# Optimization experiments

Hardware: AMD Instinct MI355X
Metric: run time of the kernel (lower is better)

The kernel has to match this reference:

```python
import jax, jax.numpy as jnp
import numpy as np

TAU = 2.0       # init_tau
VTH = 1.0       # v_threshold
VRESET = 0.0    # v_reset (hard reset)
ALPHA = 2.0     # ATan surrogate width
H = 8           # num_heads
W = 20          # attention_window
TIME_STEP = 2   # config.time_step -> global_scale uses 1000 // time_step


@jax.custom_vjp
def spike(x):
    return (x >= 0.0).astype(x.dtype)

def _spike_fwd(x):
    return (x >= 0.0).astype(x.dtype), x

def _spike_bwd(x, g):
    # ATan surrogate gradient (spikingjelly default)
    sg = (ALPHA / 2.0) / (1.0 + (jnp.pi / 2.0 * ALPHA * x) ** 2)
    return (g * sg,)

spike.defvjp(_spike_fwd, _spike_bwd)


def lif(x_seq):
    """Multi-step LIF, decay_input=False, hard reset. x_seq: [T, ...] -> spikes [T, ...]."""
    def step(v, x):
        h = v - (v - VRESET) / TAU + x          # neuronal charge (decay_input=False)
        s = spike(h - VTH)
        v_new = s * VRESET + (1.0 - s) * h      # hard reset
        return v_new, s
    _, s_seq = jax.lax.scan(step, jnp.zeros_like(x_seq[0]), x_seq)
    return s_seq


def bn(x, gamma, beta, eps=1e-5):
    # BatchNorm1d step_mode='m': stats over (T, B) per channel (training-mode stats)
    mean = x.mean(axis=(0, 1))
    var = x.var(axis=(0, 1))
    return (x - mean) * jax.lax.rsqrt(var + eps) * gamma + beta


def _shift(a, o):
    # a: [B, H, T, D]; out[..., t, :] = a[..., t + o, :], zero outside -> local band
    if o == 0:
        return a
    B_, H_, T_, D_ = a.shape
    z = jnp.zeros((B_, H_, abs(o), D_), a.dtype)
    if o > 0:
        return jnp.concatenate([a[:, :, o:, :], z], axis=2)
    return jnp.concatenate([z, a[:, :, :o, :]], axis=2)


def _forward(x, wq, wk, wv, w_mattn, w_proj, w_dw, w_pw, bn_gamma, bn_beta):
    T, B, C = x.shape
    D = C // H
    local_scale = 1.0 / np.sqrt(D * (2 * W + 1)).astype(np.float32)
    global_scale = 1.0 / np.sqrt(D * (1000 // TIME_STEP)).astype(np.float32)

    # spiking QKV: pointwise conv (kernel 1) + BN + LIF
    q = lif(bn(jnp.einsum('tbc,dc->tbd', x, wq), bn_gamma[0], bn_beta[0]))
    k = lif(bn(jnp.einsum('tbc,dc->tbd', x, wk), bn_gamma[1], bn_beta[1]))
    v = lif(bn(jnp.einsum('tbc,dc->tbd', x, wv), bn_gamma[2], bn_beta[2]))

    heads = lambda a: a.reshape(T, B, H, D).transpose(1, 2, 0, 3)   # [B,H,T,D]
    unheads = lambda a: a.transpose(2, 0, 1, 3).reshape(T, B, C)    # [T,B,C]
    qh, kh, vh = heads(q), heads(k), heads(v)

    # global spiking self-attention (no softmax): (Q K^T) V * global_scale
    attn = jnp.einsum('bhtd,bhsd->bhts', qh, kh)
    g_spk = lif(unheads(jnp.einsum('bhts,bhsd->bhtd', attn, vh) * global_scale))

    # local sliding-window attention over offsets [-W, W] (banded, no [T,T] matrix)
    out_l = jnp.zeros_like(vh)
    for o in range(-W, W + 1):
        s = jnp.einsum('bhtd,bhtd->bht', qh, _shift(kh, o))
        out_l = out_l + s[..., None] * _shift(vh, o)
    l_spk = lif(unheads(out_l * local_scale))

    # depthwise temporal conv branch on V: v_dw -> LIF -> v_pw (1x1 over heads)
    dw = jax.lax.conv_general_dilated(
        vh, w_dw, window_strides=(1, 1), padding=((4, 4), (0, 0)),
        dimension_numbers=('NCHW', 'OIHW', 'NCHW'), feature_group_count=H)
    dw_spk_h = heads(lif(unheads(dw)))
    dw_out = unheads(jnp.einsum('bhtd,gh->bgtd', dw_spk_h, w_pw))

    # merge branches, then mattn conv+BN+LIF and proj conv+BN+LIF
    y0 = lif(g_spk + l_spk + dw_out)
    y1 = lif(bn(jnp.einsum('tbc,dc->tbd', y0, w_mattn), bn_gamma[3], bn_beta[3]))
    out = lif(bn(jnp.einsum('tbc,dc->tbd', y1, w_proj), bn_gamma[4], bn_beta[4]))
    return out


def setup_inputs() -> dict:
    key = jax.random.key(0)
    ks = jax.random.split(key, 10)
    T, B, C = 500, 8, 512
    sc = 0.03
    x = jax.random.normal(ks[0], (T, B, C), jnp.float32)
    wq = jax.random.normal(ks[1], (C, C), jnp.float32) * sc
    wk = jax.random.normal(ks[2], (C, C), jnp.float32) * sc
    wv = jax.random.normal(ks[3], (C, C), jnp.float32) * sc
    w_mattn = jax.random.normal(ks[4], (C, C), jnp.float32) * sc
    w_proj = jax.random.normal(ks[5], (C, C), jnp.float32) * sc
    w_dw = jax.random.normal(ks[6], (H, 1, 9, 1), jnp.float32) * 0.3   # depthwise (9,1)
    w_pw = jax.random.normal(ks[7], (H, H), jnp.float32) * 0.3         # 1x1 over heads
    bn_gamma = jax.random.uniform(ks[8], (5, C), jnp.float32) + 0.5
    bn_beta = jax.random.normal(ks[9], (5, C), jnp.float32) * 0.1
    return {'x': x, 'wq': wq, 'wk': wk, 'wv': wv, 'w_mattn': w_mattn,
            'w_proj': w_proj, 'w_dw': w_dw, 'w_pw': w_pw,
            'bn_gamma': bn_gamma, 'bn_beta': bn_beta}


def reference(x, wq, wk, wv, w_mattn, w_proj, w_dw, w_pw, bn_gamma, bn_beta):
    return _forward(x, wq, wk, wv, w_mattn, w_proj, w_dw, w_pw, bn_gamma, bn_beta)
```

## Files before the change

### kernel.cpp

```cpp
#include <hip/hip_runtime.h>
#include <cmath>

#define TT 500
#define NTOT 2048000
#define WW 20

typedef _Float16 f16x8 __attribute__((ext_vector_type(8)));
typedef _Float16 f16x4 __attribute__((ext_vector_type(4)));
typedef float f32x4 __attribute__((ext_vector_type(4)));

#define C1SC 4.8828125e-4f
#define C2SC 2.384185791015625e-7f

__device__ __forceinline__ void gload16(const _Float16* g, _Float16* l) {
    __builtin_amdgcn_global_load_lds(
        (const __attribute__((address_space(1))) unsigned int*)g,
        (__attribute__((address_space(3))) unsigned int*)l, 16, 0, 0);
}

__global__ __launch_bounds__(256) void prep_split_k(
    const float* __restrict__ x, const float* __restrict__ wq,
    const float* __restrict__ wk, const float* __restrict__ wv,
    const float* __restrict__ wm, const float* __restrict__ wp,
    _Float16* __restrict__ X0, _Float16* __restrict__ X1, _Float16* __restrict__ X2,
    _Float16* __restrict__ Q0, _Float16* __restrict__ Q1, _Float16* __restrict__ Q2,
    _Float16* __restrict__ M0, _Float16* __restrict__ M1, _Float16* __restrict__ M2,
    _Float16* __restrict__ P0, _Float16* __restrict__ P1, _Float16* __restrict__ P2)
{
    int gid = blockIdx.x * 256 + threadIdx.x;
    const float* src;
    _Float16 *d0, *d1, *d2;
    size_t si, di;
    if (gid < 512000) {
        src = x; d0 = X0; d1 = X1; d2 = X2; si = di = (size_t)gid * 4;
    } else if (gid < 708608) {
        int g = gid - 512000;
        int s3 = g >> 16;
        src = (s3 == 0) ? wq : ((s3 == 1) ? wk : wv);
        d0 = Q0; d1 = Q1; d2 = Q2;
        si = (size_t)(g & 65535) * 4;
        di = (size_t)g * 4;
    } else if (gid < 774144) {
        int g = gid - 708608;
        src = wm; d0 = M0; d1 = M1; d2 = M2; si = di = (size_t)g * 4;
    } else {
        int g = gid - 774144;
        src = wp; d0 = P0; d1 = P1; d2 = P2; si = di = (size_t)g * 4;
    }
    float4 v = *(const float4*)(src + si);
    float f[4] = {v.x, v.y, v.z, v.w};
    f16x4 a, b, c;
#pragma unroll
    for (int i = 0; i < 4; ++i) {
        _Float16 h0 = (_Float16)f[i];
        float r1 = f[i] - (float)h0;
        _Float16 h1 = (_Float16)(r1 * 2048.0f);
        float r2 = r1 - (float)h1 * C1SC;
        _Float16 h2 = (_Float16)(r2 * 4194304.0f);
        a[i] = h0; b[i] = h1; c[i] = h2;
    }
    *(f16x4*)(d0 + di) = a;
    *(f16x4*)(d1 + di) = b;
    *(f16x4*)(d2 + di) = c;
}

__global__ __launch_bounds__(256) void gemm_f16s3_k(
    const _Float16* __restrict__ X0, const _Float16* __restrict__ X1,
    const _Float16* __restrict__ X2,
    const _Float16* __restrict__ B0g, const _Float16* __restrict__ B1g,
    const _Float16* __restrict__ B2g,
    float* __restrict__ out, float* __restrict__ colpart, int M)
{
    __shared__ __align__(16) _Float16 sA[36864];
    int tid = threadIdx.x;
    int bid = blockIdx.x;
    int xcd = bid & 7;
    int j = bid >> 3;
    int mblk = (xcd << 3) | (j & 7);
    int nblk = j >> 3;
    int mBase = mblk * 64;
    int nBase = nblk * 128;
    int wv = tid >> 6;
    int lane = tid & 63;
    int wr = wv >> 1, wc = wv & 1;
    int lg = lane >> 4, l16 = lane & 15;

    int subrow = lane >> 2;
    int s4 = lane & 3;
    int rA = (wv << 4) + subrow;
    int sl8 = (s4 ^ ((rA >> 1) & 3)) * 8;
    int mA = mBase + rA; if (mA >= M) mA = 0;
    const _Float16* gA0 = X0 + (size_t)mA * 512 + sl8;
    const _Float16* gA1 = X1 + (size_t)mA * 512 + sl8;
    const _Float16* gA2 = X2 + (size_t)mA * 512 + sl8;
    const _Float16* gB00 = B0g + (size_t)(nBase + rA) * 512 + sl8;
    const _Float16* gB01 = B0g + (size_t)(nBase + 64 + rA) * 512 + sl8;
    const _Float16* gB10 = B1g + (size_t)(nBase + rA) * 512 + sl8;
    const _Float16* gB11 = B1g + (size_t)(nBase + 64 + rA) * 512 + sl8;
    const _Float16* gB20 = B2g + (size_t)(nBase + rA) * 512 + sl8;
    const _Float16* gB21 = B2g + (size_t)(nBase + 64 + rA) * 512 + sl8;
    int wb = wv << 9;
    _Float16* lA0 = sA + wb;
    _Float16* lA1 = sA + 2048 + wb;
    _Float16* lA2 = sA + 4096 + wb;
    _Float16* lB00 = sA + 6144 + wb;
    _Float16* lB01 = sA + 8192 + wb;
    _Float16* lB10 = sA + 10240 + wb;
    _Float16* lB11 = sA + 12288 + wb;
    _Float16* lB20 = sA + 14336 + wb;
    _Float16* lB21 = sA + 16384 + wb;

    auto stage = [&](int kt, int off) {
        gload16(gA0 + kt, lA0 + off);
        gload16(gA1 + kt, lA1 + off);
        gload16(gA2 + kt, lA2 + off);
        gload16(gB00 + kt, lB00 + off);
        gload16(gB01 + kt, lB01 + off);
        gload16(gB10 + kt, lB10 + off);
        gload16(gB11 + kt, lB11 + off);
        gload16(gB20 + kt, lB20 + off);
        gload16(gB21 + kt, lB21 + off);
    };

    int sd = (lg ^ ((l16 >> 1) & 3)) * 8;

    f32x4 acc0[2][4] = {}, acc1[2][4] = {}, acc2[2][4] = {};

    stage(0, 0);
    __syncthreads();
    int cur = 0;
    for (int kt = 0; kt < 512; kt += 32) {
        int coff = cur * 18432;
        if (kt + 32 < 512) stage(kt + 32, 18432 - coff);
        f16x8 a0f[2], a1f[2], a2f[2];
#pragma unroll
        for (int i = 0; i < 2; ++i) {
            int off = (wr * 32 + i * 16 + l16) * 32 + sd + coff;
            a0f[i] = *(const f16x8*)&sA[off];
            a1f[i] = *(const f16x8*)&sA[2048 + off];
            a2f[i] = *(const f16x8*)&sA[4096 + off];
        }
#pragma unroll
        for (int jj = 0; jj < 4; ++jj) {
            int boff = 6144 + (wc * 64 + jj * 16 + l16) * 32 + sd + coff;
            f16x8 b0f = *(const f16x8*)&sA[boff];
            f16x8 b1f = *(const f16x8*)&sA[4096 + boff];
            f16x8 b2f = *(const f16x8*)&sA[8192 + boff];
#pragma unroll
            for (int i = 0; i < 2; ++i) {
                acc0[i][jj] = __builtin_amdgcn_mfma_f32_16x16x32_f16(a0f[i], b0f, acc0[i][jj], 0, 0, 0);
                acc1[i][jj] = __builtin_amdgcn_mfma_f32_16x16x32_f16(a0f[i], b1f, acc1[i][jj], 0, 0, 0);
                acc1[i][jj] = __builtin_amdgcn_mfma_f32_16x16x32_f16(a1f[i], b0f, acc1[i][jj], 0, 0, 0);
                acc2[i][jj] = __builtin_amdgcn_mfma_f32_16x16x32_f16(a1f[i], b1f, acc2[i][jj], 0, 0, 0);
                acc2[i][jj] = __builtin_amdgcn_mfma_f32_16x16x32_f16(a0f[i], b2f, acc2[i][jj], 0, 0, 0);
                acc2[i][jj] = __builtin_amdgcn_mfma_f32_16x16x32_f16(a2f[i], b0f, acc2[i][jj], 0, 0, 0);
            }
        }
        __syncthreads();
        cur ^= 1;
    }
#pragma unroll
    for (int i = 0; i < 2; ++i)
#pragma unroll
        for (int jj = 0; jj < 4; ++jj)
#pragma unroll
            for (int r = 0; r < 4; ++r)
                acc0[i][jj][r] = fmaf(C2SC, acc2[i][jj][r],
                                      fmaf(C1SC, acc1[i][jj][r], acc0[i][jj][r]));
    float* red = (float*)sA;
#pragma unroll
    for (int jj = 0; jj < 4; ++jj) {
        float s = 0.f, q = 0.f;
#pragma unroll
        for (int i = 0; i < 2; ++i)
#pragma unroll
            for (int r = 0; r < 4; ++r) {
                int mrow = mBase + wr * 32 + i * 16 + lg * 4 + r;
                float v = (mrow < M) ? acc0[i][jj][r] : 0.f;
                s += v; q = fmaf(v, v, q);
            }
        s += __shfl_xor(s, 16, 64); s += __shfl_xor(s, 32, 64);
        q += __shfl_xor(q, 16, 64); q += __shfl_xor(q, 32, 64);
        if (lane < 16) {
            int col = wc * 64 + jj * 16 + lane;
            red[(wr * 128 + col) * 2 + 0] = s;
            red[(wr * 128 + col) * 2 + 1] = q;
        }
    }
    __syncthreads();
    if (tid < 128) {
        float ss = red[tid * 2 + 0] + red[(128 + tid) * 2 + 0];
        float qq = red[tid * 2 + 1] + red[(128 + tid) * 2 + 1];
        colpart[((size_t)mblk * 1536 + nBase + tid) * 2 + 0] = ss;
        colpart[((size_t)mblk * 1536 + nBase + tid) * 2 + 1] = qq;
    }
    int wsel = nBase >> 9;
    int col0 = nBase & 511;
    float* outp = out + (size_t)wsel * NTOT;
#pragma unroll
    for (int i = 0; i < 2; ++i) {
        int m0 = mBase + wr * 32 + i * 16 + lg * 4;
#pragma unroll
        for (int jj = 0; jj < 4; ++jj) {
            int cc = col0 + wc * 64 + jj * 16 + l16;
#pragma unroll
            for (int r = 0; r < 4; ++r) {
                int m = m0 + r;
                if (m < M) outp[(size_t)m * 512 + cc] = acc0[i][jj][r];
            }
        }
    }
}

__global__ __launch_bounds__(256) void gemm_hs3_k(
    const _Float16* __restrict__ Ah,
    const _Float16* __restrict__ B0g, const _Float16* __restrict__ B1g,
    const _Float16* __restrict__ B2g,
    float* __restrict__ out, float* __restrict__ colpart, int M)
{
    __shared__ __align__(16) _Float16 sH[16384];
    int tid = threadIdx.x;
    int bid = blockIdx.x;
    int xcd = bid & 7;
    int j = bid >> 3;
    int mblk = (xcd << 3) | (j & 7);
    int nblk = j >> 3;
    int mBase = mblk * 64;
    int col0 = nblk * 64;
    int wv = tid >> 6;
    int lane = tid & 63;
    int wr = wv >> 1, wc = wv & 1;
    int lg = lane >> 4, l16 = lane & 15;

    int subrow = lane >> 2;
    int s4 = lane & 3;
    int rA = (wv << 4) + subrow;
    int sl8 = (s4 ^ ((rA >> 1) & 3)) * 8;
    int mA = mBase + rA; if (mA >= M) mA = 0;
    const _Float16* gA  = Ah  + (size_t)mA * 512 + sl8;
    const _Float16* gB0 = B0g + (size_t)(col0 + rA) * 512 + sl8;
    const _Float16* gB1 = B1g + (size_t)(col0 + rA) * 512 + sl8;
    const _Float16* gB2 = B2g + (size_t)(col0 + rA) * 512 + sl8;
    int wb = wv << 9;
    _Float16* lA  = sH + wb;
    _Float16* lB0 = sH + 2048 + wb;
    _Float16* lB1 = sH + 4096 + wb;
    _Float16* lB2 = sH + 6144 + wb;

    auto stage = [&](int kt, int off) {
        gload16(gA + kt, lA + off);
        gload16(gB0 + kt, lB0 + off);
        gload16(gB1 + kt, lB1 + off);
        gload16(gB2 + kt, lB2 + off);
    };

    int sd = (lg ^ ((l16 >> 1) & 3)) * 8;

    f32x4 acc0[2][2] = {}, acc1[2][2] = {}, acc2[2][2] = {};

    stage(0, 0);
    __syncthreads();
    int cur = 0;
    for (int kt = 0; kt < 512; kt += 32) {
        int coff = cur * 8192;
        if (kt + 32 < 512) stage(kt + 32, 8192 - coff);
        f16x8 af[2];
#pragma unroll
        for (int i = 0; i < 2; ++i)
            af[i] = *(const f16x8*)&sH[(wr * 32 + i * 16 + l16) * 32 + sd + coff];
#pragma unroll
        for (int jj = 0; jj < 2; ++jj) {
            int boff = 2048 + (wc * 32 + jj * 16 + l16) * 32 + sd + coff;
            f16x8 b0f = *(const f16x8*)&sH[boff];
            f16x8 b1f = *(const f16x8*)&sH[2048 + boff];
            f16x8 b2f = *(const f16x8*)&sH[4096 + boff];
#pragma unroll
            for (int i = 0; i < 2; ++i) {
                acc0[i][jj] = __builtin_amdgcn_mfma_f32_16x16x32_f16(af[i], b0f, acc0[i][jj], 0, 0, 0);
                acc1[i][jj] = __builtin_amdgcn_mfma_f32_16x16x32_f16(af[i], b1f, acc1[i][jj], 0, 0, 0);
                acc2[i][jj] = __builtin_amdgcn_mfma_f32_16x16x32_f16(af[i], b2f, acc2[i][jj], 0, 0, 0);
            }
        }
        __syncthreads();
        cur ^= 1;
    }
#pragma unroll
    for (int i = 0; i < 2; ++i)
#pragma unroll
        for (int jj = 0; jj < 2; ++jj)
#pragma unroll
            for (int r = 0; r < 4; ++r)
                acc0[i][jj][r] = fmaf(C2SC, acc2[i][jj][r],
                                      fmaf(C1SC, acc1[i][jj][r], acc0[i][jj][r]));
    float* red = (float*)sH;
#pragma unroll
    for (int jj = 0; jj < 2; ++jj) {
        float s = 0.f, q = 0.f;
#pragma unroll
        for (int i = 0; i < 2; ++i)
#pragma unroll
            for (int r = 0; r < 4; ++r) {
                int mrow = mBase + wr * 32 + i * 16 + lg * 4 + r;
                float v = (mrow < M) ? acc0[i][jj][r] : 0.f;
                s += v; q = fmaf(v, v, q);
            }
        s += __shfl_xor(s, 16, 64); s += __shfl_xor(s, 32, 64);
        q += __shfl_xor(q, 16, 64); q += __shfl_xor(q, 32, 64);
        if (lane < 16) {
            int col = wc * 32 + jj * 16 + lane;
            red[(wr * 64 + col) * 2 + 0] = s;
            red[(wr * 64 + col) * 2 + 1] = q;
        }
    }
    __syncthreads();
    if (tid < 64) {
        float ss = red[tid * 2 + 0] + red[(64 + tid) * 2 + 0];
        float qq = red[tid * 2 + 1] + red[(64 + tid) * 2 + 1];
        colpart[((size_t)mblk * 512 + col0 + tid) * 2 + 0] = ss;
        colpart[((size_t)mblk * 512 + col0 + tid) * 2 + 1] = qq;
    }
#pragma unroll
    for (int i = 0; i < 2; ++i) {
        int m0 = mBase + wr * 32 + i * 16 + lg * 4;
#pragma unroll
        for (int jj = 0; jj < 2; ++jj) {
            int cc = col0 + wc * 32 + jj * 16 + l16;
#pragma unroll
            for (int r = 0; r < 4; ++r) {
                int m = m0 + r;
                if (m < M) out[(size_t)m * 512 + cc] = acc0[i][jj][r];
            }
        }
    }
}

__global__ __launch_bounds__(256) void lif_seg_k(
    const float* __restrict__ pre, const float* __restrict__ colpart, int CT, int chunks,
    const float* __restrict__ gamma, const float* __restrict__ beta,
    float* __restrict__ outF, unsigned char* __restrict__ outB,
    _Float16* __restrict__ outH, int segLen, int warm)
{
    int gid = blockIdx.x * 256 + threadIdx.x;
    int tensor = gid >> 12;
    int bc = gid & 4095;
    int ch = (tensor << 9) | (bc & 511);
    double s = 0.0, s2 = 0.0;
    for (int k = 0; k < chunks; ++k) {
        s  += (double)colpart[((size_t)k * CT + ch) * 2 + 0];
        s2 += (double)colpart[((size_t)k * CT + ch) * 2 + 1];
    }
    double mean = s / 4000.0;
    double var = s2 / 4000.0 - mean * mean;
    double scd = (double)gamma[ch] / sqrt(var + 1e-5);
    float sc = (float)scd;
    float sh = (float)((double)beta[ch] - mean * scd);
    const float* q0 = pre + (size_t)tensor * NTOT + bc;
    float* oF = outF ? outF + (size_t)tensor * NTOT + bc : nullptr;
    unsigned char* oB = outB ? outB + (size_t)tensor * NTOT + bc : nullptr;
    _Float16* oH = outH ? outH + (size_t)tensor * NTOT + bc : nullptr;
    int t0 = blockIdx.y * segLen;
    int twarm = (t0 - warm > 0) ? (t0 - warm) : 0;
    int tend = (t0 + segLen < TT) ? (t0 + segLen) : TT;
    float v = 0.f;
    float b0[8];
#pragma unroll
    for (int j = 0; j < 8; ++j) {
        int tt = twarm + j;
        b0[j] = (tt < tend) ? q0[(size_t)tt * 4096] : 0.f;
    }
    for (int t = twarm; t < tend; t += 8) {
        float n0[8];
#pragma unroll
        for (int j = 0; j < 8; ++j) {
            int tt = t + 8 + j;
            n0[j] = (tt < tend) ? q0[(size_t)tt * 4096] : 0.f;
        }
#pragma unroll
        for (int j = 0; j < 8; ++j) {
            int tc = t + j;
            if (tc >= tend) break;
            float bnx = fmaf(b0[j], sc, sh);
            float h = fmaf(0.5f, v, bnx);
            float sp = (h >= 1.f) ? 1.f : 0.f;
            v = (h >= 1.f) ? 0.f : h;
            if (tc >= t0) {
                if (oB)      oB[(size_t)tc * 4096] = (unsigned char)sp;
                else if (oH) oH[(size_t)tc * 4096] = (_Float16)sp;
                else         oF[(size_t)tc * 4096] = sp;
            }
        }
#pragma unroll
        for (int j = 0; j < 8; ++j) b0[j] = n0[j];
    }
}

__global__ __launch_bounds__(256) void ktv_part_k(
    const unsigned char* __restrict__ kspk, const unsigned char* __restrict__ vspk,
    float* __restrict__ part)
{
    __shared__ __align__(16) float kb[16][64], vb[16][64];
    int bh = blockIdx.x;
    int seg = blockIdx.y;
    int t0p = seg * 125, t1p = t0p + 125;
    int b = bh >> 3, h = bh & 7;
    int tid = threadIdx.x;
    int d1b = (tid >> 4) * 4, d2b = (tid & 15) * 4;
    size_t cb = (size_t)b * 512 + h * 64;
    int sRow = tid >> 4;
    int sD = (tid & 15) * 4;
    float acc[4][4] = {};
    uchar4 pk, pv;
    auto preload = [&](int tt) {
        int t = tt + sRow;
        if (t < t1p) {
            pk = *(const uchar4*)(kspk + (size_t)t * 4096 + cb + sD);
            pv = *(const uchar4*)(vspk + (size_t)t * 4096 + cb + sD);
        } else {
            pk = make_uchar4(0, 0, 0, 0); pv = make_uchar4(0, 0, 0, 0);
        }
    };
    preload(t0p);
    for (int tt = t0p; tt < t1p; tt += 16) {
        __syncthreads();
        kb[sRow][sD + 0] = (float)pk.x; kb[sRow][sD + 1] = (float)pk.y;
        kb[sRow][sD + 2] = (float)pk.z; kb[sRow][sD + 3] = (float)pk.w;
        vb[sRow][sD + 0] = (float)pv.x; vb[sRow][sD + 1] = (float)pv.y;
        vb[sRow][sD + 2] = (float)pv.z; vb[sRow][sD + 3] = (float)pv.w;
        __syncthreads();
        preload(tt + 16);
#pragma unroll
        for (int tl = 0; tl < 16; ++tl) {
            float4 k4 = *(const float4*)&kb[tl][d1b];
            float4 v4 = *(const float4*)&vb[tl][d2b];
            float ka[4] = {k4.x, k4.y, k4.z, k4.w};
            float va[4] = {v4.x, v4.y, v4.z, v4.w};
#pragma unroll
            for (int i = 0; i < 4; ++i)
#pragma unroll
                for (int j = 0; j < 4; ++j)
                    acc[i][j] = fmaf(ka[i], va[j], acc[i][j]);
        }
    }
    size_t ob = ((size_t)seg * 64 + bh) * 4096;
#pragma unroll
    for (int i = 0; i < 4; ++i)
        *(float4*)(part + ob + (size_t)(d1b + i) * 64 + d2b) =
            make_float4(acc[i][0], acc[i][1], acc[i][2], acc[i][3]);
}

__global__ __launch_bounds__(256) void ktv_reduce_k(
    const float* __restrict__ part, float* __restrict__ ktv)
{
    int i4 = (blockIdx.x * 256 + threadIdx.x) * 4;
    float4 a = *(const float4*)(part + i4);
    float4 b = *(const float4*)(part + 262144 + i4);
    float4 c = *(const float4*)(part + 2 * 262144 + i4);
    float4 d = *(const float4*)(part + 3 * 262144 + i4);
    *(float4*)(ktv + i4) = make_float4(((a.x + b.x) + c.x) + d.x,
                                       ((a.y + b.y) + c.y) + d.y,
                                       ((a.z + b.z) + c.z) + d.z,
                                       ((a.w + b.w) + c.w) + d.w);
}

__global__ __launch_bounds__(256) void gapply_t_k(
    const unsigned char* __restrict__ sq, const float* __restrict__ ktv,
    float* __restrict__ gpre, float gscale)
{
    __shared__ float qs[10][512];
    int tid = threadIdx.x;
    int t0 = blockIdx.x * 10;
    int b = blockIdx.y;
    for (int i = tid; i < 1280; i += 256) {
        int t = i >> 7;
        int c4 = (i & 127) * 4;
        uchar4 u = *(const uchar4*)(sq + (size_t)(t0 + t) * 4096 + b * 512 + c4);
        qs[t][c4 + 0] = (float)u.x; qs[t][c4 + 1] = (float)u.y;
        qs[t][c4 + 2] = (float)u.z; qs[t][c4 + 3] = (float)u.w;
    }
    __syncthreads();
#pragma unroll
    for (int half = 0; half < 2; ++half) {
        int c = tid + half * 256;
        int h = c >> 6, dcol = c & 63;
        const float* kt = ktv + ((size_t)(b * 8 + h) * 64) * 64 + dcol;
        float acc[10] = {};
        for (int d1 = 0; d1 < 64; ++d1) {
            float kv = kt[(size_t)d1 * 64];
#pragma unroll
            for (int t = 0; t < 10; ++t)
                acc[t] = fmaf(qs[t][h * 64 + d1], kv, acc[t]);
        }
#pragma unroll
        for (int t = 0; t < 10; ++t)
            gpre[(size_t)(t0 + t) * 4096 + b * 512 + c] = acc[t] * gscale;
    }
}

__global__ __launch_bounds__(256) void local_k(
    const unsigned char* __restrict__ qspk, const unsigned char* __restrict__ kspk,
    const unsigned char* __restrict__ vspk, float* __restrict__ lpre, float lscale)
{
    __shared__ __align__(16) float qs[32][68];
    __shared__ __align__(16) float ks[72][68];
    __shared__ __align__(16) float vs[72][68];
    __shared__ float sm[32][72];
    int t0 = blockIdx.x * 32;
    int bh = blockIdx.y;
    int b = bh >> 3, h = bh & 7;
    int tid = threadIdx.x;
    size_t cb = (size_t)b * 512 + h * 64;

    for (int i = tid; i < 512; i += 256) {
        int r = i >> 4, d4 = (i & 15) * 4;
        int t = t0 + r;
        if (t < TT) {
            uchar4 u = *(const uchar4*)(qspk + (size_t)t * 4096 + cb + d4);
            qs[r][d4 + 0] = (float)u.x; qs[r][d4 + 1] = (float)u.y;
            qs[r][d4 + 2] = (float)u.z; qs[r][d4 + 3] = (float)u.w;
        } else {
            qs[r][d4 + 0] = 0.f; qs[r][d4 + 1] = 0.f; qs[r][d4 + 2] = 0.f; qs[r][d4 + 3] = 0.f;
        }
    }
    for (int i = tid; i < 1152; i += 256) {
        int r = i >> 4, d4 = (i & 15) * 4;
        int u_ = t0 - WW + r;
        if (u_ >= 0 && u_ < TT) {
            uchar4 uk = *(const uchar4*)(kspk + (size_t)u_ * 4096 + cb + d4);
            uchar4 uv = *(const uchar4*)(vspk + (size_t)u_ * 4096 + cb + d4);
            ks[r][d4 + 0] = (float)uk.x; ks[r][d4 + 1] = (float)uk.y;
            ks[r][d4 + 2] = (float)uk.z; ks[r][d4 + 3] = (float)uk.w;
            vs[r][d4 + 0] = (float)uv.x; vs[r][d4 + 1] = (float)uv.y;
            vs[r][d4 + 2] = (float)uv.z; vs[r][d4 + 3] = (float)uv.w;
        } else {
            ks[r][d4 + 0] = 0.f; ks[r][d4 + 1] = 0.f; ks[r][d4 + 2] = 0.f; ks[r][d4 + 3] = 0.f;
            vs[r][d4 + 0] = 0.f; vs[r][d4 + 1] = 0.f; vs[r][d4 + 2] = 0.f; vs[r][d4 + 3] = 0.f;
        }
    }
    __syncthreads();

    int tA = tid >> 3;
    int ug = tid & 7;
    float4 qreg[16];
#pragma unroll
    for (int i = 0; i < 16; ++i) qreg[i] = *(const float4*)&qs[tA][i * 4];
#pragma unroll
    for (int ui = 0; ui < 9; ++ui) {
        int u = ug + ui * 8;
        float acc = 0.f;
#pragma unroll
        for (int i = 0; i < 16; ++i) {
            float4 k4 = *(const float4*)&ks[u][i * 4];
            acc = fmaf(qreg[i].x, k4.x, acc);
            acc = fmaf(qreg[i].y, k4.y, acc);
            acc = fmaf(qreg[i].z, k4.z, acc);
            acc = fmaf(qreg[i].w, k4.w, acc);
        }
        sm[tA][u] = acc;
    }
    __syncthreads();

#pragma unroll
    for (int oi = 0; oi < 2; ++oi) {
        int idx = tid + oi * 256;
        int t = idx >> 4;
        int dg = (idx & 15) * 4;
        float4 acc = make_float4(0.f, 0.f, 0.f, 0.f);
        for (int o = 0; o < 41; ++o) {
            int u = t + o;
            float s = sm[t][u];
            float4 v4 = *(const float4*)&vs[u][dg];
            acc.x = fmaf(s, v4.x, acc.x);
            acc.y = fmaf(s, v4.y, acc.y);
            acc.z = fmaf(s, v4.z, acc.z);
            acc.w = fmaf(s, v4.w, acc.w);
        }
        int tg = t0 + t;
        if (tg < TT) {
            acc.x *= lscale; acc.y *= lscale; acc.z *= lscale; acc.w *= lscale;
            *(float4*)(lpre + (size_t)tg * 4096 + cb + dg) = acc;
        }
    }
}

__global__ __launch_bounds__(256) void branch_y0_k(
    const float* __restrict__ gpre, const float* __restrict__ lpre,
    const unsigned char* __restrict__ sv, const float* __restrict__ wdw,
    const float* __restrict__ wpw, _Float16* __restrict__ sy0,
    int segLen, int warm)
{
    int tid = threadIdx.x;
    int wave = tid >> 6, lane = tid & 63;
    int gw = blockIdx.x * 4 + wave;
    int b = gw >> 3, dg = gw & 7;
    int h = lane >> 3, dl = lane & 7;
    int c = h * 64 + dg * 8 + dl;
    int base = b * 512 + c;
    float w9[9];
#pragma unroll
    for (int j = 0; j < 9; ++j) w9[j] = wdw[h * 9 + j];
    float w8[8];
#pragma unroll
    for (int j = 0; j < 8; ++j) w8[j] = wpw[h * 8 + j];
    int t0 = blockIdx.y * segLen;
    int twarm = (t0 - warm > 0) ? (t0 - warm) : 0;
    int tend = (t0 + segLen < TT) ? (t0 + segLen) : TT;
    float vg = 0.f, vl = 0.f, vd = 0.f, vy = 0.f;
    float win[12];
#pragma unroll
    for (int i = 0; i < 12; ++i) {
        int tt = twarm - 4 + i;
        win[i] = (tt >= 0 && tt < TT) ? (float)sv[(size_t)tt * 4096 + base] : 0.f;
    }
    float pg[4], pl[4], pv[4];
    auto pref = [&](int t) {
#pragma unroll
        for (int j = 0; j < 4; ++j) {
            int tt = t + j;
            bool in = tt < tend;
            pg[j] = in ? gpre[(size_t)tt * 4096 + base] : 0.f;
            pl[j] = in ? lpre[(size_t)tt * 4096 + base] : 0.f;
            int tv = t + 8 + j;
            pv[j] = (tv < TT) ? (float)sv[(size_t)tv * 4096 + base] : 0.f;
        }
    };
    pref(twarm);
    for (int t = twarm; t < tend; t += 4) {
        float cg[4], cl[4], cv[4];
#pragma unroll
        for (int j = 0; j < 4; ++j) { cg[j] = pg[j]; cl[j] = pl[j]; cv[j] = pv[j]; }
        pref(t + 4);
#pragma unroll
        for (int j = 0; j < 4; ++j) {
            int tc = t + j;
            if (tc >= tend) break;
            float x = 0.f;
#pragma unroll
            for (int q = 0; q < 9; ++q) x = fmaf(w9[q], win[j + q], x);
            float hd = fmaf(0.5f, vd, x);
            float sd = (hd >= 1.f) ? 1.f : 0.f;
            vd = (hd >= 1.f) ? 0.f : hd;
            float hg = fmaf(0.5f, vg, cg[j]);
            float sg = (hg >= 1.f) ? 1.f : 0.f;
            vg = (hg >= 1.f) ? 0.f : hg;
            float hl = fmaf(0.5f, vl, cl[j]);
            float sl = (hl >= 1.f) ? 1.f : 0.f;
            vl = (hl >= 1.f) ? 0.f : hl;
            float mix = 0.f;
#pragma unroll
            for (int h2 = 0; h2 < 8; ++h2)
                mix = fmaf(w8[h2], __shfl(sd, h2 * 8 + dl, 64), mix);
            float xy = (sg + sl) + mix;
            float hy = fmaf(0.5f, vy, xy);
            float sy = (hy >= 1.f) ? 1.f : 0.f;
            vy = (hy >= 1.f) ? 0.f : hy;
            if (tc >= t0) sy0[(size_t)tc * 4096 + base] = (_Float16)sy;
        }
#pragma unroll
        for (int i = 0; i < 8; ++i) win[i] = win[i + 4];
#pragma unroll
        for (int i = 0; i < 4; ++i) win[8 + i] = cv[i];
    }
}

extern "C" void kernel_launch(void* const* d_in, const int* in_sizes, int n_in,
                              void* d_out, int out_size, void* d_ws, size_t ws_size,
                              hipStream_t stream)
{
    const float* x       = (const float*)d_in[0];
    const float* wq      = (const float*)d_in[1];
    const float* wk      = (const float*)d_in[2];
    const float* wv      = (const float*)d_in[3];
    const float* w_mattn = (const float*)d_in[4];
    const float* w_proj  = (const float*)d_in[5];
    const float* w_dw    = (const float*)d_in[6];
    const float* w_pw    = (const float*)d_in[7];
    const float* bn_g    = (const float*)d_in[8];
    const float* bn_b    = (const float*)d_in[9];
    float* out = (float*)d_out;
    float* ws = (float*)d_ws;

    float gs32 = (float)std::sqrt((double)(64 * 500));
    float gscale = (float)(1.0 / (double)gs32);
    float ls32 = (float)std::sqrt((double)(64 * 41));
    float lscale = (float)(1.0 / (double)ls32);
    const int M = TT * 8;

    float* S0 = ws;
    float* S1 = ws + (size_t)NTOT;
    float* S2 = ws + 2 * (size_t)NTOT;
    float* part4   = ws + 3 * (size_t)NTOT;
    float* ktvBuf  = part4 + 4 * 262144;
    float* colpart = ktvBuf + 262144;
    unsigned char* spk = (unsigned char*)(colpart + 196608);
    unsigned char* sq  = spk;
    unsigned char* sk  = spk + (size_t)NTOT;
    unsigned char* sv  = spk + 2 * (size_t)NTOT;
    _Float16* sy0h = (_Float16*)(spk + 3 * (size_t)NTOT);
    _Float16* sy1h = (_Float16*)spk;
    _Float16* X0 = (_Float16*)spk;
    _Float16* X1 = X0 + (size_t)NTOT;
    _Float16* X2 = X1 + (size_t)NTOT;
    _Float16* Wm0 = (_Float16*)(spk + 6 * (size_t)NTOT);
    _Float16* Wm1 = Wm0 + 262144;
    _Float16* Wm2 = Wm1 + 262144;
    _Float16* Wp0 = Wm2 + 262144;
    _Float16* Wp1 = Wp0 + 262144;
    _Float16* Wp2 = Wp1 + 262144;
    _Float16* Wq0 = (_Float16*)part4;
    _Float16* Wq1 = Wq0 + 786432;
    _Float16* Wq2 = Wq1 + 786432;

    prep_split_k<<<3280, 256, 0, stream>>>(x, wq, wk, wv, w_mattn, w_proj,
                                           X0, X1, X2, Wq0, Wq1, Wq2,
                                           Wm0, Wm1, Wm2, Wp0, Wp1, Wp2);
    gemm_f16s3_k<<<768, 256, 0, stream>>>(X0, X1, X2, Wq0, Wq1, Wq2, S0, colpart, M);
    lif_seg_k<<<dim3(48, 10), 256, 0, stream>>>(S0, colpart, 1536, 64, bn_g, bn_b,
                                                nullptr, sq, nullptr, 50, 64);
    ktv_part_k<<<dim3(64, 4), 256, 0, stream>>>(sk, sv, part4);
    ktv_reduce_k<<<256, 256, 0, stream>>>(part4, ktvBuf);
    gapply_t_k<<<dim3(50, 8), 256, 0, stream>>>(sq, ktvBuf, S0, gscale);
    local_k<<<dim3(16, 64), 256, 0, stream>>>(sq, sk, sv, S1, lscale);
    branch_y0_k<<<dim3(16, 20), 256, 0, stream>>>(S0, S1, sv, w_dw, w_pw, sy0h, 25, 64);
    gemm_hs3_k<<<512, 256, 0, stream>>>(sy0h, Wm0, Wm1, Wm2, S2, colpart, M);
    lif_seg_k<<<dim3(16, 20), 256, 0, stream>>>(S2, colpart, 512, 64, bn_g + 1536,
                                                bn_b + 1536, nullptr, nullptr, sy1h, 25, 64);
    gemm_hs3_k<<<512, 256, 0, stream>>>(sy1h, Wp0, Wp1, Wp2, S0, colpart, M);
    lif_seg_k<<<dim3(16, 20), 256, 0, stream>>>(S0, colpart, 512, 64, bn_g + 2048,
                                                bn_b + 2048, out, nullptr, nullptr, 25, 64);

    (void)in_sizes; (void)n_in; (void)out_size; (void)ws_size;
}
```

Measured before the change: 331.7 us.

## Stage branch_y0 inputs through double-buffered LDS via async global-to-LDS loads

Replaces the per-thread register prefetch of gpre, lpre and spike values in branch_y0_k with cooperative global_load_lds staging into double-buffered shared memory, eight timesteps at a time, using a swizzled column mapping so each load is wide and contiguous. The goal is to turn strided 4-byte per-lane loads into 16-byte vectorized transfers and overlap the next chunk's loads with the current sequential LIF recurrence. It adds block-wide barriers each chunk and extra LDS use, and the window update now shifts one element per step. The staged loads may read past tend or TT at the tail, which could touch out-of-range addresses.

```diff
diff --git a/kernel.cpp b/kernel.cpp
--- a/kernel.cpp
+++ b/kernel.cpp
@@ -16,6 +16,16 @@
     __builtin_amdgcn_global_load_lds(
         (const __attribute__((address_space(1))) unsigned int*)g,
         (__attribute__((address_space(3))) unsigned int*)l, 16, 0, 0);
+}
+__device__ __forceinline__ void gload16f(const float* g, float* l) {
+    __builtin_amdgcn_global_load_lds(
+        (const __attribute__((address_space(1))) unsigned int*)g,
+        (__attribute__((address_space(3))) unsigned int*)l, 16, 0, 0);
+}
+__device__ __forceinline__ void gload4b(const unsigned char* g, unsigned char* l) {
+    __builtin_amdgcn_global_load_lds(
+        (const __attribute__((address_space(1))) unsigned int*)g,
+        (__attribute__((address_space(3))) unsigned int*)l, 4, 0, 0);
 }
 
 __global__ __launch_bounds__(256) void prep_split_k(
@@ -588,13 +598,32 @@
     const float* __restrict__ wpw, _Float16* __restrict__ sy0,
     int segLen, int warm)
 {
+    __shared__ __align__(16) float gb[2][8][256];
+    __shared__ __align__(16) float lb[2][8][256];
+    __shared__ __align__(16) unsigned char vbuf[2][8][256];
     int tid = threadIdx.x;
     int wave = tid >> 6, lane = tid & 63;
-    int gw = blockIdx.x * 4 + wave;
-    int b = gw >> 3, dg = gw & 7;
+    int gw0 = blockIdx.x * 4;
+    int b = gw0 >> 3;
+    int dg0 = gw0 & 7;
     int h = lane >> 3, dl = lane & 7;
+    int dg = dg0 + wave;
     int c = h * 64 + dg * 8 + dl;
     int base = b * 512 + c;
+    int p = h * 32 + (((wave + h) & 3) << 3) + dl;
+
+    int rowS[2], gcol[2];
+#pragma unroll
+    for (int v = 0; v < 2; ++v) {
+        int f = tid + (v << 8);
+        rowS[v] = f >> 6;
+        int jj = f & 63;
+        int hj = jj >> 3;
+        int sj = (jj >> 1) & 3;
+        int wj = (sj - hj) & 3;
+        gcol[v] = b * 512 + hj * 64 + dg0 * 8 + (wj << 3) + ((jj & 1) << 2);
+    }
+
     float w9[9];
 #pragma unroll
     for (int j = 0; j < 9; ++j) w9[j] = wdw[h * 9 + j];
@@ -604,6 +633,25 @@
     int t0 = blockIdx.y * segLen;
     int twarm = (t0 - warm > 0) ? (t0 - warm) : 0;
     int tend = (t0 + segLen < TT) ? (t0 + segLen) : TT;
+
+    auto stageGL = [&](int ct, int bi) {
+#pragma unroll
+        for (int v = 0; v < 2; ++v) {
+            size_t ga = (size_t)(ct + rowS[v]) * 4096 + gcol[v];
+            int lo = (v << 10) + (wave << 8);
+            gload16f(gpre + ga, &gb[bi][0][0] + lo);
+            gload16f(lpre + ga, &lb[bi][0][0] + lo);
+        }
+    };
+    auto stageV = [&](int ct, int bi) {
+#pragma unroll
+        for (int v = 0; v < 2; ++v) {
+            size_t ga = (size_t)(ct + rowS[v]) * 4096 + gcol[v];
+            int lo = (v << 10) + (wave << 8);
+            gload4b(sv + ga, &vbuf[bi][0][0] + lo);
+        }
+    };
+
     float vg = 0.f, vl = 0.f, vd = 0.f, vy = 0.f;
     float win[12];
 #pragma unroll
@@ -611,38 +659,29 @@
         int tt = twarm - 4 + i;
         win[i] = (tt >= 0 && tt < TT) ? (float)sv[(size_t)tt * 4096 + base] : 0.f;
     }
-    float pg[4], pl[4], pv[4];
-    auto pref = [&](int t) {
-#pragma unroll
-        for (int j = 0; j < 4; ++j) {
-            int tt = t + j;
-            bool in = tt < tend;
-            pg[j] = in ? gpre[(size_t)tt * 4096 + base] : 0.f;
-            pl[j] = in ? lpre[(size_t)tt * 4096 + base] : 0.f;
-            int tv = t + 8 + j;
-            pv[j] = (tv < TT) ? (float)sv[(size_t)tv * 4096 + base] : 0.f;
-        }
-    };
-    pref(twarm);
-    for (int t = twarm; t < tend; t += 4) {
-        float cg[4], cl[4], cv[4];
-#pragma unroll
-        for (int j = 0; j < 4; ++j) { cg[j] = pg[j]; cl[j] = pl[j]; cv[j] = pv[j]; }
-        pref(t + 4);
-#pragma unroll
-        for (int j = 0; j < 4; ++j) {
-            int tc = t + j;
+    stageGL(twarm, 0);
+    stageV(twarm + 8, 0);
+    __syncthreads();
+    int cur = 0;
+    for (int T0 = twarm; T0 < tend; T0 += 8) {
+        if (T0 + 8 < tend) { stageGL(T0 + 8, cur ^ 1); stageV(T0 + 16, cur ^ 1); }
+#pragma unroll
+        for (int r = 0; r < 8; ++r) {
+            int tc = T0 + r;
             if (tc >= tend) break;
+            float cg = gb[cur][r][p];
+            float cl = lb[cur][r][p];
+            float nv = (tc + 8 < TT) ? (float)vbuf[cur][r][p] : 0.f;
             float x = 0.f;
 #pragma unroll
-            for (int q = 0; q < 9; ++q) x = fmaf(w9[q], win[j + q], x);
+            for (int q = 0; q < 9; ++q) x = fmaf(w9[q], win[q], x);
             float hd = fmaf(0.5f, vd, x);
             float sd = (hd >= 1.f) ? 1.f : 0.f;
             vd = (hd >= 1.f) ? 0.f : hd;
-            float hg = fmaf(0.5f, vg, cg[j]);
+            float hg = fmaf(0.5f, vg, cg);
             float sg = (hg >= 1.f) ? 1.f : 0.f;
             vg = (hg >= 1.f) ? 0.f : hg;
-            float hl = fmaf(0.5f, vl, cl[j]);
+            float hl = fmaf(0.5f, vl, cl);
             float sl = (hl >= 1.f) ? 1.f : 0.f;
             vl = (hl >= 1.f) ? 0.f : hl;
             float mix = 0.f;
@@ -654,11 +693,12 @@
             float sy = (hy >= 1.f) ? 1.f : 0.f;
             vy = (hy >= 1.f) ? 0.f : hy;
             if (tc >= t0) sy0[(size_t)tc * 4096 + base] = (_Float16)sy;
-        }
-#pragma unroll
-        for (int i = 0; i < 8; ++i) win[i] = win[i + 4];
-#pragma unroll
-        for (int i = 0; i < 4; ++i) win[8 + i] = cv[i];
+#pragma unroll
+            for (int i2 = 0; i2 < 11; ++i2) win[i2] = win[i2 + 1];
+            win[11] = nv;
+        }
+        __syncthreads();
+        cur ^= 1;
     }
 }
 
```

Result: faster. 315.4 us (-4.9%).
